# Optimization experiments

Hardware: AMD Instinct MI355X
Metric: run time of the kernel (lower is better)

The kernel has to match this reference:

```python
import jax, jax.numpy as jnp
import numpy as np

N = 100000   # nodes
E = 500000   # edges per relation
R = 3        # relations (etypes)
L = 2        # layers
F = 300      # input features
H = 256      # hidden
C = 23       # classes


def setup_inputs() -> dict:
    key = jax.random.key(0)
    ks = jax.random.split(key, 12)
    s = 0.05
    return {
        "x": jax.random.normal(ks[0], (N, F), jnp.float32),
        "edge_src": jax.random.randint(ks[1], (R, E), 0, N, dtype=jnp.int32),
        "edge_dst": jax.random.randint(ks[2], (R, E), 0, N, dtype=jnp.int32),
        "W_feat": jax.random.normal(ks[3], (F, H), jnp.float32) * s,
        "b_feat": jnp.zeros((H,), jnp.float32),
        "g_feat": jnp.ones((H,), jnp.float32),
        "beta_feat": jnp.zeros((H,), jnp.float32),
        "gcn_W": jax.random.normal(ks[4], (L, R, H, H), jnp.float32) * s,
        "gcn_b": jnp.zeros((L, R, H), jnp.float32),
        "skip_W": jax.random.normal(ks[5], (L, H, H), jnp.float32) * s,
        "skip_b": jnp.zeros((L, H), jnp.float32),
        "bn_g": jnp.ones((L, H), jnp.float32),
        "bn_b": jnp.zeros((L, H), jnp.float32),
        "W_c1": jax.random.normal(ks[6], (H, H), jnp.float32) * s,
        "b_c1": jnp.zeros((H,), jnp.float32),
        "g_c": jnp.ones((H,), jnp.float32),
        "beta_c": jnp.zeros((H,), jnp.float32),
        "W_c2": jax.random.normal(ks[7], (H, C), jnp.float32) * s,
        "b_c2": jnp.zeros((C,), jnp.float32),
    }


def _bn(h, g, b):
    # BatchNorm1d, training-mode batch stats (biased var), eps=1e-5
    m = h.mean(0)
    v = jnp.mean((h - m) ** 2, 0)
    return g * (h - m) * jax.lax.rsqrt(v + 1e-5) + b


def _het_forward(x, edge_src, edge_dst, W_feat, b_feat, g_feat, beta_feat,
                 gcn_W, gcn_b, skip_W, skip_b, bn_g, bn_b,
                 W_c1, b_c1, g_c, beta_c, W_c2, b_c2):
    seg = jax.ops.segment_sum
    ones = jnp.ones((E,), jnp.float32)
    # feat_reduce: Linear + BN + ReLU
    h = jax.nn.relu(_bn(x @ W_feat + b_feat, g_feat, beta_feat))  # [N, H]
    for l in range(L):
        h_res = h @ skip_W[l] + skip_b[l]
        rel = []
        for r in range(R):  # per-relation GraphConv (DGL norm='both')
            src, dst = edge_src[r], edge_dst[r]
            dout = jnp.clip(seg(ones, src, num_segments=N), 1.0, None)
            din = jnp.clip(seg(ones, dst, num_segments=N), 1.0, None)
            xs = h * jax.lax.rsqrt(dout)[:, None]          # src-normalize
            m = seg(xs[src], dst, num_segments=N)          # gather-scatter
            m = m * jax.lax.rsqrt(din)[:, None]            # dst-normalize
            rel.append(m @ gcn_W[l, r] + gcn_b[l, r])
        h = jnp.mean(jnp.stack(rel, 0), 0)  # het_combine='mean'
        h = h + h_res
        h = jax.nn.leaky_relu(_bn(h, bn_g[l], bn_b[l]), 0.01)
        # dropout is identity in eval mode
    # classification head
    h = jax.nn.relu(_bn(h @ W_c1 + b_c1, g_c, beta_c))
    return h @ W_c2 + b_c2  # [N, C]


def reference(x, edge_src, edge_dst, W_feat, b_feat, g_feat, beta_feat,
              gcn_W, gcn_b, skip_W, skip_b, bn_g, bn_b,
              W_c1, b_c1, g_c, beta_c, W_c2, b_c2):
    return _het_forward(x, edge_src, edge_dst, W_feat, b_feat, g_feat,
                        beta_feat, gcn_W, gcn_b, skip_W, skip_b, bn_g, bn_b,
                        W_c1, b_c1, g_c, beta_c, W_c2, b_c2)
```

## Files before the change

kernel.cpp:

```cpp
#include <hip/hip_runtime.h>

#define NN 100000
#define EE 500000
#define RR 3
#define LL 2
#define FF 300
#define HH 256
#define CC 23
#define MPAD 100096
#define SCHUNK 2048
#define SNB ((NN + SCHUNK - 1) / SCHUNK)

static inline int cdiv_h(int a, int b) { return (a + b - 1) / b; }

typedef __attribute__((ext_vector_type(8))) short bf16x8;
typedef __attribute__((ext_vector_type(4))) float f32x4;
typedef __attribute__((ext_vector_type(4))) unsigned short u16x4;

__device__ inline unsigned short f2bf(float f) {
    union { float f; unsigned int u; } v; v.f = f;
    unsigned int r = v.u + 0x7fff + ((v.u >> 16) & 1);
    return (unsigned short)(r >> 16);
}
__device__ inline float bf2f(unsigned short u) {
    union { unsigned int u; float f; } v; v.u = ((unsigned int)u) << 16;
    return v.f;
}
__device__ inline void gl_lds16(const void* g, void* l) {
    __builtin_amdgcn_global_load_lds((const __attribute__((address_space(1))) unsigned int*)g,
                                     (__attribute__((address_space(3))) unsigned int*)l,
                                     16, 0, 0);
}

__global__ void hist_kernel(const int* __restrict__ src, const int* __restrict__ dst,
                            int* __restrict__ cnt_out, int* __restrict__ cnt_in,
                            int RE, int Eper) {
    int i = blockIdx.x * blockDim.x + threadIdx.x;
    if (i >= RE) return;
    int r = i / Eper;
    atomicAdd(&cnt_out[r * NN + src[i]], 1);
    atomicAdd(&cnt_in[r * NN + dst[i]], 1);
}

__global__ void rs_kernel(const int* __restrict__ cnt_out, const int* __restrict__ cnt_in,
                          float* __restrict__ rs_out, float* __restrict__ rs_in, int total) {
    int i = blockIdx.x * blockDim.x + threadIdx.x;
    if (i >= total) return;
    rs_out[i] = rsqrtf(fmaxf((float)cnt_out[i], 1.0f));
    rs_in[i]  = rsqrtf(fmaxf((float)cnt_in[i], 1.0f));
}

__global__ __launch_bounds__(256) void scan_a(const int* __restrict__ cnt, int* __restrict__ bsum) {
    int r = blockIdx.y, b = blockIdx.x, t = threadIdx.x;
    const int* c = cnt + (size_t)r * NN;
    int base = b * SCHUNK;
    int s = 0;
    for (int i = t; i < SCHUNK; i += 256) {
        int idx = base + i;
        if (idx < NN) s += c[idx];
    }
#pragma unroll
    for (int o = 1; o < 64; o <<= 1) s += __shfl_xor(s, o);
    __shared__ int sh[4];
    if ((t & 63) == 0) sh[t >> 6] = s;
    __syncthreads();
    if (t == 0) bsum[r * SNB + b] = sh[0] + sh[1] + sh[2] + sh[3];
}

__global__ void scan_b(int* __restrict__ bsum, int* __restrict__ offs) {
    int r = threadIdx.x;
    if (r >= RR) return;
    int* bs = bsum + r * SNB;
    int run = 0;
    for (int i = 0; i < SNB; i++) { int v = bs[i]; bs[i] = run; run += v; }
    offs[(size_t)r * (NN + 1) + NN] = run;
}

__global__ __launch_bounds__(256) void scan_c(const int* __restrict__ cnt, const int* __restrict__ bsum,
                                              int* __restrict__ offs, int* __restrict__ cur) {
    int r = blockIdx.y, b = blockIdx.x, t = threadIdx.x;
    const int* c = cnt + (size_t)r * NN;
    int base = b * SCHUNK + t * 8;
    int v[8]; int s = 0;
#pragma unroll
    for (int j = 0; j < 8; j++) {
        int idx = base + j;
        v[j] = (idx < NN) ? c[idx] : 0;
        s += v[j];
    }
    __shared__ int sh[256];
    sh[t] = s;
    __syncthreads();
    for (int d = 1; d < 256; d <<= 1) {
        int x = (t >= d) ? sh[t - d] : 0;
        __syncthreads();
        sh[t] += x;
        __syncthreads();
    }
    int run = sh[t] - s + bsum[r * SNB + b];
    int* orow = offs + (size_t)r * (NN + 1);
    int* crow = cur + (size_t)r * NN;
#pragma unroll
    for (int j = 0; j < 8; j++) {
        int idx = base + j;
        if (idx < NN) { orow[idx] = run; crow[idx] = run; }
        run += v[j];
    }
}

__global__ void fill_kernel(const int* __restrict__ src, const int* __restrict__ dst,
                            const float* __restrict__ rs_out,
                            int* __restrict__ cur, int2* __restrict__ srcw,
                            int RE, int Eper) {
    int i = blockIdx.x * blockDim.x + threadIdx.x;
    if (i >= RE) return;
    int r = i / Eper;
    int d = dst[i];
    int s = src[i];
    float w = rs_out[r * NN + s];
    int pos = atomicAdd(&cur[r * NN + d], 1);
    srcw[(size_t)r * Eper + pos] = make_int2(s, __float_as_int(w));
}

__global__ void convert_x(const float* __restrict__ x, unsigned short* __restrict__ xpad) {
    int row = blockIdx.x;
    int col = threadIdx.x;
    float v = (row < NN && col < FF) ? x[(size_t)row * FF + col] : 0.f;
    xpad[(size_t)row * 320 + col] = f2bf(v);
}

__global__ void wprep_feat(const float* __restrict__ W, unsigned short* __restrict__ Bt) {
    int n = blockIdx.x;
    int k = threadIdx.x;
    float v = (k < FF) ? W[(size_t)k * HH + n] : 0.f;
    Bt[(size_t)n * 320 + k] = f2bf(v);
}

__global__ void wprep_layer(const float* __restrict__ skipW, const float* __restrict__ gcnW,
                            unsigned short* __restrict__ Bt) {
    int idx = blockIdx.x * blockDim.x + threadIdx.x;
    int n = idx >> 10, k = idx & 1023;
    int seg = k >> 8, k2 = k & 255;
    float v = (seg == 0) ? skipW[(size_t)k2 * HH + n]
                         : gcnW[(size_t)(seg - 1) * HH * HH + (size_t)k2 * HH + n] * (1.0f / 3.0f);
    Bt[(size_t)n * 1024 + k] = f2bf(v);
}

__global__ void bias_layer(const float* __restrict__ skip_b, const float* __restrict__ gcn_b,
                           float* __restrict__ bias) {
    int t = threadIdx.x;
    bias[t] = skip_b[t] + (gcn_b[t] + gcn_b[HH + t] + gcn_b[2 * HH + t]) * (1.0f / 3.0f);
}

__global__ void wprep_c1(const float* __restrict__ W, unsigned short* __restrict__ Bt) {
    int idx = blockIdx.x * blockDim.x + threadIdx.x;
    int n = idx >> 8, k = idx & 255;
    Bt[(size_t)n * HH + k] = f2bf(W[(size_t)k * HH + n]);
}

__global__ void wprep_c2(const float* __restrict__ W, unsigned short* __restrict__ Bt) {
    int n = blockIdx.x;
    int k = threadIdx.x;
    float v = (n < CC) ? W[(size_t)k * CC + n] : 0.f;
    Bt[(size_t)n * HH + k] = f2bf(v);
}

__global__ __launch_bounds__(256) void agg_bf16(unsigned short* __restrict__ hcat,
                                                const int* __restrict__ offs_all,
                                                const int2* __restrict__ srcw_all,
                                                const float* __restrict__ rs_in_all) {
    int r = blockIdx.y;
    const int* offs = offs_all + (size_t)r * (NN + 1);
    const int2* srcw = srcw_all + (size_t)r * EE;
    const float* rs_i = rs_in_all + (size_t)r * NN;
    int wave = threadIdx.x >> 6;
    int lane = threadIdx.x & 63;
    int node = blockIdx.x * 4 + wave;
    if (node >= NN) return;
    int s0 = __builtin_amdgcn_readfirstlane(offs[node]);
    int s1 = __builtin_amdgcn_readfirstlane(offs[node + 1]);
    int cnt = s1 - s0;
    const int2* ew = srcw + s0;
    const unsigned short* hb = hcat + lane * 4;
    float a0 = 0.f, a1 = 0.f, a2 = 0.f, a3 = 0.f;
    int k = 0;
    for (; k + 8 <= cnt; k += 8) {
        int2 e[8];
#pragma unroll
        for (int q = 0; q < 8; q++) e[q] = ew[k + q];
        ushort4 hv[8];
#pragma unroll
        for (int q = 0; q < 8; q++) hv[q] = *(const ushort4*)(hb + (size_t)e[q].x * 1024);
#pragma unroll
        for (int q = 0; q < 8; q++) {
            float u = __int_as_float(e[q].y);
            a0 += u * bf2f(hv[q].x); a1 += u * bf2f(hv[q].y);
            a2 += u * bf2f(hv[q].z); a3 += u * bf2f(hv[q].w);
        }
    }
    if (k + 4 <= cnt) {
        int2 e[4];
#pragma unroll
        for (int q = 0; q < 4; q++) e[q] = ew[k + q];
        ushort4 hv[4];
#pragma unroll
        for (int q = 0; q < 4; q++) hv[q] = *(const ushort4*)(hb + (size_t)e[q].x * 1024);
#pragma unroll
        for (int q = 0; q < 4; q++) {
            float u = __int_as_float(e[q].y);
            a0 += u * bf2f(hv[q].x); a1 += u * bf2f(hv[q].y);
            a2 += u * bf2f(hv[q].z); a3 += u * bf2f(hv[q].w);
        }
        k += 4;
    }
    int rem = cnt - k;
    if (rem > 0) {
        int2 e[3];
#pragma unroll
        for (int q = 0; q < 3; q++) {
            int kk = k + q; if (kk > cnt - 1) kk = cnt - 1;
            e[q] = ew[kk];
        }
        ushort4 hv[3];
#pragma unroll
        for (int q = 0; q < 3; q++) hv[q] = *(const ushort4*)(hb + (size_t)e[q].x * 1024);
        float u0 = __int_as_float(e[0].y);
        float u1 = rem > 1 ? __int_as_float(e[1].y) : 0.f;
        float u2 = rem > 2 ? __int_as_float(e[2].y) : 0.f;
        a0 += u0 * bf2f(hv[0].x) + u1 * bf2f(hv[1].x) + u2 * bf2f(hv[2].x);
        a1 += u0 * bf2f(hv[0].y) + u1 * bf2f(hv[1].y) + u2 * bf2f(hv[2].y);
        a2 += u0 * bf2f(hv[0].z) + u1 * bf2f(hv[1].z) + u2 * bf2f(hv[2].z);
        a3 += u0 * bf2f(hv[0].w) + u1 * bf2f(hv[1].w) + u2 * bf2f(hv[2].w);
    }
    float wi = rs_i[node];
    u16x4 o;
    o.x = f2bf(a0 * wi); o.y = f2bf(a1 * wi);
    o.z = f2bf(a2 * wi); o.w = f2bf(a3 * wi);
    __builtin_nontemporal_store(o, (u16x4*)(hcat + (size_t)node * 1024 + 256 * (r + 1) + lane * 4));
}

__global__ __launch_bounds__(512, 4) void mfma_gemm(const unsigned short* __restrict__ A, int ldA,
                                                    const unsigned short* __restrict__ Bt,
                                                    const float* __restrict__ bias,
                                                    void* __restrict__ Cv, int ldC,
                                                    int Nstore, int K, int c_bf16,
                                                    float* __restrict__ stats) {
    __shared__ unsigned short ldsA[2][128 * 32];
    __shared__ unsigned short ldsB[2][256 * 32];
    int tid = threadIdx.x;
    int w = tid >> 6, lane = tid & 63;
    int quad = lane >> 4, lr = lane & 15;
    int bm = blockIdx.y * 128;
    int wm = w >> 2, wn = w & 3;
    int lrow = lane >> 2;
    int lslot = lane & 3;

    f32x4 acc[4][4];
#pragma unroll
    for (int i = 0; i < 4; i++)
#pragma unroll
        for (int j = 0; j < 4; j++) acc[i][j] = (f32x4){0.f, 0.f, 0.f, 0.f};

    for (int k0 = 0; k0 < K; k0 += 64) {
        int rA = w * 16 + lrow;
        int cgA = lslot ^ ((rA >> 1) & 3);
#pragma unroll
        for (int h = 0; h < 2; h++) {
            gl_lds16(A + (size_t)(bm + rA) * ldA + k0 + h * 32 + cgA * 8,
                     &ldsA[h][w * 512]);
#pragma unroll
            for (int c = 0; c < 2; c++) {
                int cc = w * 2 + c;
                int rB = cc * 16 + lrow;
                int cgB = lslot ^ ((rB >> 1) & 3);
                gl_lds16(Bt + (size_t)rB * K + k0 + h * 32 + cgB * 8,
                         &ldsB[h][cc * 512]);
            }
        }
        __syncthreads();
#pragma unroll
        for (int h = 0; h < 2; h++) {
            bf16x8 af[4], bfr[4];
#pragma unroll
            for (int i = 0; i < 4; i++) {
                int r = wm * 64 + i * 16 + lr;
                int s = quad ^ ((r >> 1) & 3);
                af[i] = *(const bf16x8*)&ldsA[h][r * 32 + s * 8];
            }
#pragma unroll
            for (int j = 0; j < 4; j++) {
                int n = wn * 64 + j * 16 + lr;
                int s = quad ^ ((n >> 1) & 3);
                bfr[j] = *(const bf16x8*)&ldsB[h][n * 32 + s * 8];
            }
#pragma unroll
            for (int i = 0; i < 4; i++)
#pragma unroll
                for (int j = 0; j < 4; j++)
                    acc[i][j] = __builtin_amdgcn_mfma_f32_16x16x32_bf16(af[i], bfr[j], acc[i][j], 0, 0, 0);
        }
        __syncthreads();
    }

    float* Cf = (float*)Cv;
    unsigned short* Cb = (unsigned short*)Cv;
#pragma unroll
    for (int j = 0; j < 4; j++) {
        int col = wn * 64 + j * 16 + lr;
        if (col >= Nstore) continue;
        float bv = bias ? bias[col] : 0.f;
        float ssum = 0.f, ssq = 0.f;
#pragma unroll
        for (int i = 0; i < 4; i++) {
#pragma unroll
            for (int v = 0; v < 4; v++) {
                int row = bm + wm * 64 + i * 16 + quad * 4 + v;
                if (row < NN) {
                    float val = acc[i][j][v] + bv;
                    if (c_bf16) Cb[(size_t)row * ldC + col] = f2bf(val);
                    else        Cf[(size_t)row * ldC + col] = val;
                    ssum += val; ssq += val * val;
                }
            }
        }
        if (stats) {
            ssum += __shfl_xor(ssum, 16); ssum += __shfl_xor(ssum, 32);
            ssq  += __shfl_xor(ssq, 16);  ssq  += __shfl_xor(ssq, 32);
            if (quad == 0) {
                atomicAdd(&stats[col], ssum);
                atomicAdd(&stats[HH + col], ssq);
            }
        }
    }
}

__global__ void bn_coef(const float* __restrict__ stats, const float* __restrict__ g,
                        const float* __restrict__ b, float* __restrict__ coef, float invM) {
    int c = threadIdx.x;
    float mean = stats[c] * invM;
    float var = stats[HH + c] * invM - mean * mean;
    float inv = rsqrtf(var + 1e-5f);
    float sc = g[c] * inv;
    coef[c] = sc;
    coef[HH + c] = b[c] - mean * sc;
}

__global__ __launch_bounds__(256) void bn_apply_v(const unsigned short* __restrict__ Z,
                                                  const float* __restrict__ coef,
                                                  unsigned short* __restrict__ out, int act) {
    int idx = blockIdx.x * blockDim.x + threadIdx.x;
    if (idx >= NN * 32) return;
    int row = idx >> 5, cg = (idx & 31) * 8;
    union { uint4 u; unsigned short s[8]; } zin, zo;
    zin.u = *(const uint4*)(Z + (size_t)row * HH + cg);
    f32x4 sc0 = *(const f32x4*)(coef + cg);
    f32x4 sc1 = *(const f32x4*)(coef + cg + 4);
    f32x4 sh0 = *(const f32x4*)(coef + HH + cg);
    f32x4 sh1 = *(const f32x4*)(coef + HH + cg + 4);
#pragma unroll
    for (int j = 0; j < 8; j++) {
        float sc = (j < 4) ? sc0[j] : sc1[j - 4];
        float sh = (j < 4) ? sh0[j] : sh1[j - 4];
        float v = bf2f(zin.s[j]) * sc + sh;
        if (act == 1) v = fmaxf(v, 0.f);
        else v = (v < 0.f) ? 0.01f * v : v;
        zo.s[j] = f2bf(v);
    }
    *(uint4*)(out + (size_t)row * 1024 + cg) = zo.u;
}

extern "C" void kernel_launch(void* const* d_in, const int* in_sizes, int n_in,
                              void* d_out, int out_size, void* d_ws, size_t ws_size,
                              hipStream_t stream) {
    const float* x        = (const float*)d_in[0];
    const int*   esrc     = (const int*)d_in[1];
    const int*   edst     = (const int*)d_in[2];
    const float* W_feat   = (const float*)d_in[3];
    const float* b_feat   = (const float*)d_in[4];
    const float* g_feat   = (const float*)d_in[5];
    const float* beta_feat= (const float*)d_in[6];
    const float* gcn_W    = (const float*)d_in[7];
    const float* gcn_b    = (const float*)d_in[8];
    const float* skip_W   = (const float*)d_in[9];
    const float* skip_b   = (const float*)d_in[10];
    const float* bn_g     = (const float*)d_in[11];
    const float* bn_b     = (const float*)d_in[12];
    const float* W_c1     = (const float*)d_in[13];
    const float* b_c1     = (const float*)d_in[14];
    const float* g_c      = (const float*)d_in[15];
    const float* beta_c   = (const float*)d_in[16];
    const float* W_c2     = (const float*)d_in[17];
    const float* b_c2     = (const float*)d_in[18];
    float* out = (float*)d_out;
    (void)in_sizes; (void)n_in; (void)out_size; (void)ws_size;

    char* w = (char*)d_ws;
    size_t off = 0;
    auto alloc = [&](size_t bytes) { void* p = w + off; off += (bytes + 255) & ~(size_t)255; return p; };
    unsigned short* hcat = (unsigned short*)alloc((size_t)MPAD * 1024 * 2);
    unsigned short* xpad = hcat;
    unsigned short* c_acc = (unsigned short*)alloc((size_t)NN * HH * 2);
    float* f_stats = (float*)alloc(4 * 2 * HH * 4);
    float* f_coef  = (float*)alloc(2 * HH * 4);
    float* f_rs_out = (float*)alloc((size_t)RR * NN * 4);
    float* f_rs_in  = (float*)alloc((size_t)RR * NN * 4);
    int* i_cnt_out = (int*)alloc((size_t)RR * NN * 4);
    int* i_cnt_in  = (int*)alloc((size_t)RR * NN * 4);
    int* i_off     = (int*)alloc((size_t)RR * (NN + 1) * 4);
    int* i_cur     = (int*)alloc((size_t)RR * NN * 4);
    int2* i_srcw   = (int2*)alloc((size_t)RR * EE * 8);
    int* i_bsum    = (int*)alloc((size_t)RR * SNB * 4);
    unsigned short* Bt_feat = (unsigned short*)alloc(256 * 320 * 2);
    unsigned short* Bt_l0   = (unsigned short*)alloc(256 * 1024 * 2);
    unsigned short* Bt_l1   = (unsigned short*)alloc(256 * 1024 * 2);
    unsigned short* Bt_c1   = (unsigned short*)alloc(256 * 256 * 2);
    unsigned short* Bt_c2   = (unsigned short*)alloc(256 * 256 * 2);
    float* bias_l0 = (float*)alloc(HH * 4);
    float* bias_l1 = (float*)alloc(HH * 4);

    const float invM = 1.0f / (float)NN;
    const int RE = RR * EE;

    (void)hipMemsetAsync(i_cnt_out, 0, (size_t)RR * NN * 4, stream);
    (void)hipMemsetAsync(i_cnt_in, 0, (size_t)RR * NN * 4, stream);
    (void)hipMemsetAsync(f_stats, 0, 4 * 2 * HH * 4, stream);
    hist_kernel<<<cdiv_h(RE, 256), 256, 0, stream>>>(esrc, edst, i_cnt_out, i_cnt_in, RE, EE);
    rs_kernel<<<cdiv_h(RR * NN, 256), 256, 0, stream>>>(i_cnt_out, i_cnt_in, f_rs_out, f_rs_in, RR * NN);
    scan_a<<<dim3(SNB, RR), 256, 0, stream>>>(i_cnt_in, i_bsum);
    scan_b<<<1, 64, 0, stream>>>(i_bsum, i_off);
    scan_c<<<dim3(SNB, RR), 256, 0, stream>>>(i_cnt_in, i_bsum, i_off, i_cur);
    fill_kernel<<<cdiv_h(RE, 256), 256, 0, stream>>>(esrc, edst, f_rs_out, i_cur, i_srcw, RE, EE);

    convert_x<<<MPAD, 320, 0, stream>>>(x, xpad);
    wprep_feat<<<256, 320, 0, stream>>>(W_feat, Bt_feat);
    wprep_layer<<<1024, 256, 0, stream>>>(skip_W, gcn_W, Bt_l0);
    wprep_layer<<<1024, 256, 0, stream>>>(skip_W + (size_t)HH * HH, gcn_W + (size_t)RR * HH * HH, Bt_l1);
    bias_layer<<<1, 256, 0, stream>>>(skip_b, gcn_b, bias_l0);
    bias_layer<<<1, 256, 0, stream>>>(skip_b + HH, gcn_b + (size_t)RR * HH, bias_l1);
    wprep_c1<<<256, 256, 0, stream>>>(W_c1, Bt_c1);
    wprep_c2<<<256, 256, 0, stream>>>(W_c2, Bt_c2);

    dim3 grid_G(1, MPAD / 128);
    const int nblk_a = cdiv_h(NN * 32, 256);
    float* st0 = f_stats;
    float* st1 = f_stats + 2 * HH;
    float* st2 = f_stats + 4 * HH;
    float* st3 = f_stats + 6 * HH;

    mfma_gemm<<<grid_G, 512, 0, stream>>>(xpad, 320, Bt_feat, b_feat, c_acc, HH, HH, 320, 1, st0);
    bn_coef<<<1, 256, 0, stream>>>(st0, g_feat, beta_feat, f_coef, invM);
    bn_apply_v<<<nblk_a, 256, 0, stream>>>(c_acc, f_coef, hcat, 1);

    for (int l = 0; l < LL; l++) {
        agg_bf16<<<dim3(cdiv_h(NN, 4), RR), 256, 0, stream>>>(hcat, i_off, i_srcw, f_rs_in);
        float* st = l ? st2 : st1;
        mfma_gemm<<<grid_G, 512, 0, stream>>>(hcat, 1024, l ? Bt_l1 : Bt_l0,
                                              l ? bias_l1 : bias_l0, c_acc, HH, HH, 1024, 1, st);
        bn_coef<<<1, 256, 0, stream>>>(st, bn_g + (size_t)l * HH, bn_b + (size_t)l * HH, f_coef, invM);
        bn_apply_v<<<nblk_a, 256, 0, stream>>>(c_acc, f_coef, hcat, 2);
    }

    mfma_gemm<<<grid_G, 512, 0, stream>>>(hcat, 1024, Bt_c1, b_c1, c_acc, HH, HH, 256, 1, st3);
    bn_coef<<<1, 256, 0, stream>>>(st3, g_c, beta_c, f_coef, invM);
    bn_apply_v<<<nblk_a, 256, 0, stream>>>(c_acc, f_coef, hcat + 256, 1);
    mfma_gemm<<<grid_G, 512, 0, stream>>>(hcat + 256, 1024, Bt_c2, b_c2, out, CC, CC, 256, 0, nullptr);
}
```

Measured before the change: 1.206 ms.

## Double-buffer GEMM LDS tiles, stage bf16 epilogue through LDS, vectorize x conversion

The MFMA GEMM now double-buffers its A/B LDS tiles, issuing the next K-tile's global-to-LDS loads before computing the current one, with one barrier per iteration instead of two. The bf16 output epilogue writes through a padded LDS tile and then stores full rows with 16-byte vector writes, replacing scattered 2-byte stores. The fp32 path skips the unused stats code. convert_x is also rewritten to read float4 and write ushort4 per thread. The doubled LDS footprint lowers the occupancy hint from 4 to 2 blocks per SM, which may reduce latency hiding.

```diff
diff --git a/kernel.cpp b/kernel.cpp
--- a/kernel.cpp
+++ b/kernel.cpp
@@ -122,11 +122,18 @@
     srcw[(size_t)r * Eper + pos] = make_int2(s, __float_as_int(w));
 }
 
-__global__ void convert_x(const float* __restrict__ x, unsigned short* __restrict__ xpad) {
-    int row = blockIdx.x;
-    int col = threadIdx.x;
-    float v = (row < NN && col < FF) ? x[(size_t)row * FF + col] : 0.f;
-    xpad[(size_t)row * 320 + col] = f2bf(v);
+__global__ __launch_bounds__(256) void convert_x(const float* __restrict__ x, unsigned short* __restrict__ xpad) {
+    int idx = blockIdx.x * blockDim.x + threadIdx.x;
+    if (idx >= MPAD * 80) return;
+    int row = idx / 80, c4 = (idx - row * 80) * 4;
+    ushort4 o;
+    if (row < NN && c4 + 3 < FF) {
+        float4 v = *(const float4*)(x + (size_t)row * FF + c4);
+        o.x = f2bf(v.x); o.y = f2bf(v.y); o.z = f2bf(v.z); o.w = f2bf(v.w);
+    } else {
+        o.x = 0; o.y = 0; o.z = 0; o.w = 0;
+    }
+    *(ushort4*)(xpad + (size_t)row * 320 + c4) = o;
 }
 
 __global__ void wprep_feat(const float* __restrict__ W, unsigned short* __restrict__ Bt) {
@@ -239,14 +246,13 @@
     __builtin_nontemporal_store(o, (u16x4*)(hcat + (size_t)node * 1024 + 256 * (r + 1) + lane * 4));
 }
 
-__global__ __launch_bounds__(512, 4) void mfma_gemm(const unsigned short* __restrict__ A, int ldA,
+__global__ __launch_bounds__(512, 2) void mfma_gemm(const unsigned short* __restrict__ A, int ldA,
                                                     const unsigned short* __restrict__ Bt,
                                                     const float* __restrict__ bias,
                                                     void* __restrict__ Cv, int ldC,
                                                     int Nstore, int K, int c_bf16,
                                                     float* __restrict__ stats) {
-    __shared__ unsigned short ldsA[2][128 * 32];
-    __shared__ unsigned short ldsB[2][256 * 32];
+    __shared__ unsigned short lds[2][24576];
     int tid = threadIdx.x;
     int w = tid >> 6, lane = tid & 63;
     int quad = lane >> 4, lr = lane & 15;
@@ -261,23 +267,35 @@
 #pragma unroll
         for (int j = 0; j < 4; j++) acc[i][j] = (f32x4){0.f, 0.f, 0.f, 0.f};
 
-    for (int k0 = 0; k0 < K; k0 += 64) {
+    const int NT = K >> 6;
+
+    auto stage = [&](int bi, int t) {
+        int k0 = t << 6;
         int rA = w * 16 + lrow;
         int cgA = lslot ^ ((rA >> 1) & 3);
 #pragma unroll
         for (int h = 0; h < 2; h++) {
             gl_lds16(A + (size_t)(bm + rA) * ldA + k0 + h * 32 + cgA * 8,
-                     &ldsA[h][w * 512]);
+                     &lds[bi][h * 4096 + w * 512]);
 #pragma unroll
             for (int c = 0; c < 2; c++) {
                 int cc = w * 2 + c;
                 int rB = cc * 16 + lrow;
                 int cgB = lslot ^ ((rB >> 1) & 3);
                 gl_lds16(Bt + (size_t)rB * K + k0 + h * 32 + cgB * 8,
-                         &ldsB[h][cc * 512]);
+                         &lds[bi][8192 + h * 8192 + cc * 512]);
             }
         }
-        __syncthreads();
+    };
+
+    stage(0, 0);
+    asm volatile("s_waitcnt vmcnt(0)" ::: "memory");
+    __builtin_amdgcn_s_barrier();
+    asm volatile("" ::: "memory");
+
+    int cur = 0;
+    for (int t = 0; t < NT; t++) {
+        if (t + 1 < NT) stage(cur ^ 1, t + 1);
 #pragma unroll
         for (int h = 0; h < 2; h++) {
             bf16x8 af[4], bfr[4];
@@ -285,13 +303,13 @@
             for (int i = 0; i < 4; i++) {
                 int r = wm * 64 + i * 16 + lr;
                 int s = quad ^ ((r >> 1) & 3);
-                af[i] = *(const bf16x8*)&ldsA[h][r * 32 + s * 8];
+                af[i] = *(const bf16x8*)&lds[cur][h * 4096 + r * 32 + s * 8];
             }
 #pragma unroll
             for (int j = 0; j < 4; j++) {
                 int n = wn * 64 + j * 16 + lr;
                 int s = quad ^ ((n >> 1) & 3);
-                bfr[j] = *(const bf16x8*)&ldsB[h][n * 32 + s * 8];
+                bfr[j] = *(const bf16x8*)&lds[cur][8192 + h * 8192 + n * 32 + s * 8];
             }
 #pragma unroll
             for (int i = 0; i < 4; i++)
@@ -299,36 +317,65 @@
                 for (int j = 0; j < 4; j++)
                     acc[i][j] = __builtin_amdgcn_mfma_f32_16x16x32_bf16(af[i], bfr[j], acc[i][j], 0, 0, 0);
         }
-        __syncthreads();
-    }
-
-    float* Cf = (float*)Cv;
-    unsigned short* Cb = (unsigned short*)Cv;
-#pragma unroll
-    for (int j = 0; j < 4; j++) {
-        int col = wn * 64 + j * 16 + lr;
-        if (col >= Nstore) continue;
-        float bv = bias ? bias[col] : 0.f;
-        float ssum = 0.f, ssq = 0.f;
-#pragma unroll
-        for (int i = 0; i < 4; i++) {
-#pragma unroll
-            for (int v = 0; v < 4; v++) {
-                int row = bm + wm * 64 + i * 16 + quad * 4 + v;
-                if (row < NN) {
+        if (t + 1 < NT) {
+            asm volatile("s_waitcnt vmcnt(0)" ::: "memory");
+            __builtin_amdgcn_s_barrier();
+            asm volatile("" ::: "memory");
+        }
+        cur ^= 1;
+    }
+
+    __syncthreads();
+
+    if (c_bf16) {
+        unsigned short* ldsC = &lds[0][0];
+#pragma unroll
+        for (int j = 0; j < 4; j++) {
+            int col = wn * 64 + j * 16 + lr;
+            float bv = bias ? bias[col] : 0.f;
+            float ssum = 0.f, ssq = 0.f;
+#pragma unroll
+            for (int i = 0; i < 4; i++) {
+#pragma unroll
+                for (int v = 0; v < 4; v++) {
+                    int row = wm * 64 + i * 16 + quad * 4 + v;
                     float val = acc[i][j][v] + bv;
-                    if (c_bf16) Cb[(size_t)row * ldC + col] = f2bf(val);
-                    else        Cf[(size_t)row * ldC + col] = val;
-                    ssum += val; ssq += val * val;
+                    ldsC[row * 264 + col] = f2bf(val);
+                    if (bm + row < NN) { ssum += val; ssq += val * val; }
                 }
             }
-        }
-        if (stats) {
-            ssum += __shfl_xor(ssum, 16); ssum += __shfl_xor(ssum, 32);
-            ssq  += __shfl_xor(ssq, 16);  ssq  += __shfl_xor(ssq, 32);
-            if (quad == 0) {
-                atomicAdd(&stats[col], ssum);
-                atomicAdd(&stats[HH + col], ssq);
+            if (stats) {
+                ssum += __shfl_xor(ssum, 16); ssum += __shfl_xor(ssum, 32);
+                ssq  += __shfl_xor(ssq, 16);  ssq  += __shfl_xor(ssq, 32);
+                if (quad == 0) {
+                    atomicAdd(&stats[col], ssum);
+                    atomicAdd(&stats[HH + col], ssq);
+                }
+            }
+        }
+        __syncthreads();
+        int row = tid >> 2, seg = tid & 3;
+        if (bm + row < NN) {
+            const unsigned short* srcp = ldsC + row * 264 + seg * 64;
+            unsigned short* dstp = (unsigned short*)Cv + (size_t)(bm + row) * ldC + seg * 64;
+#pragma unroll
+            for (int q = 0; q < 8; q++)
+                *(uint4*)(dstp + q * 8) = *(const uint4*)(srcp + q * 8);
+        }
+    } else {
+        float* Cf = (float*)Cv;
+#pragma unroll
+        for (int j = 0; j < 4; j++) {
+            int col = wn * 64 + j * 16 + lr;
+            if (col >= Nstore) continue;
+            float bv = bias ? bias[col] : 0.f;
+#pragma unroll
+            for (int i = 0; i < 4; i++) {
+#pragma unroll
+                for (int v = 0; v < 4; v++) {
+                    int row = bm + wm * 64 + i * 16 + quad * 4 + v;
+                    if (row < NN) Cf[(size_t)row * ldC + col] = acc[i][j][v] + bv;
+                }
             }
         }
     }
@@ -431,7 +478,7 @@
     scan_c<<<dim3(SNB, RR), 256, 0, stream>>>(i_cnt_in, i_bsum, i_off, i_cur);
     fill_kernel<<<cdiv_h(RE, 256), 256, 0, stream>>>(esrc, edst, f_rs_out, i_cur, i_srcw, RE, EE);
 
-    convert_x<<<MPAD, 320, 0, stream>>>(x, xpad);
+    convert_x<<<cdiv_h(MPAD * 80, 256), 256, 0, stream>>>(x, xpad);
     wprep_feat<<<256, 320, 0, stream>>>(W_feat, Bt_feat);
     wprep_layer<<<1024, 256, 0, stream>>>(skip_W, gcn_W, Bt_l0);
     wprep_layer<<<1024, 256, 0, stream>>>(skip_W + (size_t)HH * HH, gcn_W + (size_t)RR * HH * HH, Bt_l1);
```

Result: no change. 1.212 ms (+0.4%).
